# Performance work log

Measured on AMD Instinct MI355X. Metric: run time of the kernel, lower is better.

Reference implementation:

```python
import jax, jax.numpy as jnp
import numpy as np

N = 100_000   # nodes
E = 1_600_000 # edges
IN = 128
OUT = 64
L = 3         # n_layers


def setup_inputs() -> dict:
    key = jax.random.key(0)
    ks = jax.random.split(key, 4)
    x = jax.random.normal(ks[0], (N, IN), dtype=jnp.float32)
    edge_index = jax.random.randint(ks[1], (2, E), 0, N, dtype=jnp.int64)
    # Glorot-ish init like torch Linear default
    s0 = 1.0 / np.sqrt(IN)
    W0 = jax.random.uniform(ks[2], (IN, OUT), jnp.float32, -s0, s0)
    b0 = jnp.zeros((OUT,), jnp.float32)
    so = 1.0 / np.sqrt(OUT)
    Ws = jax.random.uniform(ks[3], (L - 1, OUT, OUT), jnp.float32, -so, so)
    bs = jnp.zeros((L - 1, OUT), jnp.float32)
    return {"x": x, "edge_index": edge_index, "W0": W0, "b0": b0, "Ws": Ws, "bs": bs}


def _gcn_conv(x, src, dst, norm, W, b):
    # dense transform then degree-normalized scatter-add over edges (incl. self-loops)
    h = x @ W                                  # [N, out]
    msg = h[src] * norm[:, None]               # [E+N, out]
    out = jax.ops.segment_sum(msg, dst, num_segments=N)
    return out + b


def reference(x, edge_index, W0, b0, Ws, bs):
    loops = jnp.arange(N, dtype=edge_index.dtype)
    src = jnp.concatenate([edge_index[0], loops])  # source nodes (x_j)
    dst = jnp.concatenate([edge_index[1], loops])  # aggregation targets
    # symmetric GCN normalization: deg over A+I, norm = d^-1/2[src]*d^-1/2[dst]
    deg = jax.ops.segment_sum(jnp.ones(src.shape, x.dtype), dst, num_segments=N)
    dinv = jnp.where(deg > 0, jax.lax.rsqrt(deg), jnp.zeros((), x.dtype))
    norm = dinv[src] * dinv[dst]

    x_temp = _gcn_conv(x, src, dst, norm, W0, b0)
    h = x_temp
    for i in range(L - 1):  # fixed small layer loop
        h = jax.nn.relu(_gcn_conv(h, src, dst, norm, Ws[i], bs[i]))
    return h + x_temp  # sum_res residual
```

## Files before the change

kernel.cpp:

```cpp
#include <hip/hip_runtime.h>


#define LB 8
#define BKN 256
#define CHUNK 2048
#define CAP 8192
#define PADS 3
#define CAPCOL (CAP + BKN * PADS)

typedef unsigned short ushort_t;
typedef __attribute__((ext_vector_type(8))) short bf16x8;
typedef __attribute__((ext_vector_type(4))) float f32x4;

__device__ __forceinline__ unsigned f2bf(float f) {
    unsigned u = __builtin_bit_cast(unsigned, f);
    return (u + 0x7FFFu + ((u >> 16) & 1u)) >> 16;
}
__device__ __forceinline__ float bf2f(ushort_t h) {
    unsigned u = ((unsigned)h) << 16;
    return __builtin_bit_cast(float, u);
}
__device__ __forceinline__ float bflo(unsigned u) {
    return __builtin_bit_cast(float, u << 16);
}
__device__ __forceinline__ float bfhi(unsigned u) {
    return __builtin_bit_cast(float, u & 0xFFFF0000u);
}

__device__ int detect_f64(const int* ei, int E, int* sflag) {
    if (threadIdx.x == 0) *sflag = 0;
    __syncthreads();
    const unsigned* raw = (const unsigned*)ei;
    int dwords = min(2 * E, 4096);
    int any = 0;
    for (int i = threadIdx.x; i < dwords; i += blockDim.x)
        if ((i & 1) && raw[i]) any = 1;
    if (any) atomicOr(sflag, 1);
    __syncthreads();
    return !*sflag;
}

__global__ __launch_bounds__(256) void k_scatter(
        const int* __restrict__ ei, int E,
        int* __restrict__ bucketCursor, unsigned int* __restrict__ packed) {
    __shared__ int hist[512];
    __shared__ int base[512];
    __shared__ int sflag;
    int f64 = detect_f64(ei, E, &sflag);
    int b0 = blockIdx.x * CHUNK;
    int n = min(CHUNK, E - b0);
    for (int i = threadIdx.x; i < 512; i += 256) hist[i] = 0;
    __syncthreads();
    for (int i = threadIdx.x; i < n; i += 256) {
        int e = b0 + i;
        int d = f64 ? ei[2 * (E + e)] : ei[E + e];
        atomicAdd(&hist[d >> LB], 1);
    }
    __syncthreads();
    for (int i = threadIdx.x; i < 512; i += 256) {
        int c = hist[i];
        base[i] = c ? atomicAdd(&bucketCursor[i], c) : 0;
        hist[i] = 0;
    }
    __syncthreads();
    for (int i = threadIdx.x; i < n; i += 256) {
        int e = b0 + i;
        int d = f64 ? ei[2 * (E + e)] : ei[E + e];
        int s = f64 ? ei[2 * e] : ei[e];
        int bk = d >> LB;
        int pos = bk * CAP + base[bk] + atomicAdd(&hist[bk], 1);
        packed[pos] = ((unsigned)s << LB) | (unsigned)(d & (BKN - 1));
    }
}

__global__ __launch_bounds__(256) void k_sort(
        const unsigned int* __restrict__ packed, const int* __restrict__ bucketCursor,
        int* __restrict__ col, int2* __restrict__ rp2, float* __restrict__ dinv,
        ushort_t* __restrict__ hs, int N) {
    __shared__ int hist[BKN];
    __shared__ int s[BKN];
    __shared__ int cur[BKN];
    int tid = threadIdx.x;
    int b = blockIdx.x;
    int start = b * CAP;
    int end = start + bucketCursor[b];
    hist[tid] = 0;
    __syncthreads();
    for (int e = start + tid; e < end; e += 256)
        atomicAdd(&hist[packed[e] & (BKN - 1)], 1);
    __syncthreads();
    int v = hist[tid];
    int pv = (v + PADS) & ~PADS;
    s[tid] = pv;
    __syncthreads();
    for (int off = 1; off < 256; off <<= 1) {
        int x = (tid >= off) ? s[tid - off] : 0;
        __syncthreads();
        if (tid >= off) s[tid] += x;
        __syncthreads();
    }
    int excl = s[tid] - pv;
    int st = b * CAPCOL + excl;
    cur[tid] = st;
    int node = (b << LB) + tid;
    if (node < N) {
        rp2[node] = make_int2(st, st + pv);
        dinv[node] = rsqrtf((float)(v + 1));
        for (int i = v; i < pv; i++) col[st + i] = N;
    }
    if (b == 0 && tid < 64) hs[(size_t)N * 64 + tid] = 0;
    __syncthreads();
    for (int e = start + tid; e < end; e += 256) {
        unsigned pvk = packed[e];
        int pos = atomicAdd(&cur[pvk & (BKN - 1)], 1);
        col[pos] = (int)(pvk >> LB);
    }
}

__global__ __launch_bounds__(256) void k_gemm1(
        const float* __restrict__ A, const float* __restrict__ W,
        const float* __restrict__ dinv, ushort_t* __restrict__ out, int nrows) {
    const int K = 128;
    __shared__ ushort_t sWT[64 * (K + 8)];
    int tid = threadIdx.x;
    for (int i = tid; i < K * 64; i += 256) {
        int n = i & 63, k = i >> 6;
        sWT[n * (K + 8) + k] = (ushort_t)f2bf(W[i]);
    }
    __syncthreads();
    int wave = tid >> 6, lane = tid & 63;
    int quad = lane >> 4, l16 = lane & 15;
    int rowBase = blockIdx.x * 128 + wave * 32;
    f32x4 acc[2][4];
#pragma unroll
    for (int r = 0; r < 2; r++)
#pragma unroll
        for (int c = 0; c < 4; c++) acc[r][c] = (f32x4){0.f, 0.f, 0.f, 0.f};
#pragma unroll
    for (int chunk = 0; chunk < K / 32; chunk++) {
        bf16x8 afr[2];
#pragma unroll
        for (int r = 0; r < 2; r++) {
            int row = rowBase + r * 16 + l16;
            if (row >= nrows) row = nrows - 1;
            const float* ap = A + (size_t)row * K + chunk * 32 + quad * 8;
            float4 v0 = *(const float4*)ap;
            float4 v1 = *(const float4*)(ap + 4);
            bf16x8 a;
            a[0] = (short)f2bf(v0.x); a[1] = (short)f2bf(v0.y);
            a[2] = (short)f2bf(v0.z); a[3] = (short)f2bf(v0.w);
            a[4] = (short)f2bf(v1.x); a[5] = (short)f2bf(v1.y);
            a[6] = (short)f2bf(v1.z); a[7] = (short)f2bf(v1.w);
            afr[r] = a;
        }
#pragma unroll
        for (int c = 0; c < 4; c++) {
            bf16x8 bfr = __builtin_bit_cast(
                bf16x8,
                *(const uint4*)&sWT[(c * 16 + l16) * (K + 8) + chunk * 32 + quad * 8]);
#pragma unroll
            for (int r = 0; r < 2; r++)
                acc[r][c] = __builtin_amdgcn_mfma_f32_16x16x32_bf16(
                    afr[r], bfr, acc[r][c], 0, 0, 0);
        }
    }
#pragma unroll
    for (int r = 0; r < 2; r++)
#pragma unroll
        for (int i = 0; i < 4; i++) {
            int row = rowBase + r * 16 + quad * 4 + i;
            if (row < nrows) {
                float sc = dinv[row];
#pragma unroll
                for (int c = 0; c < 4; c++)
                    out[(size_t)row * 64 + c * 16 + l16] =
                        (ushort_t)f2bf(acc[r][c][i] * sc);
            }
        }
}

__global__ __launch_bounds__(256) void k_gemm64(
        const ushort_t* __restrict__ A, const float* __restrict__ W,
        const float* __restrict__ dinv, ushort_t* __restrict__ out, int nrows) {
    const int K = 64;
    __shared__ ushort_t sWT[64 * (K + 8)];
    int tid = threadIdx.x;
    for (int i = tid; i < K * 64; i += 256) {
        int n = i & 63, k = i >> 6;
        sWT[n * (K + 8) + k] = (ushort_t)f2bf(W[i]);
    }
    __syncthreads();
    int wave = tid >> 6, lane = tid & 63;
    int quad = lane >> 4, l16 = lane & 15;
    int rowBase = blockIdx.x * 128 + wave * 32;
    f32x4 acc[2][4];
#pragma unroll
    for (int r = 0; r < 2; r++)
#pragma unroll
        for (int c = 0; c < 4; c++) acc[r][c] = (f32x4){0.f, 0.f, 0.f, 0.f};
#pragma unroll
    for (int chunk = 0; chunk < K / 32; chunk++) {
        bf16x8 afr[2];
#pragma unroll
        for (int r = 0; r < 2; r++) {
            int row = rowBase + r * 16 + l16;
            if (row >= nrows) row = nrows - 1;
            const ushort_t* ap = A + (size_t)row * K + chunk * 32 + quad * 8;
            afr[r] = __builtin_bit_cast(bf16x8, *(const uint4*)ap);
        }
#pragma unroll
        for (int c = 0; c < 4; c++) {
            bf16x8 bfr = __builtin_bit_cast(
                bf16x8,
                *(const uint4*)&sWT[(c * 16 + l16) * (K + 8) + chunk * 32 + quad * 8]);
#pragma unroll
            for (int r = 0; r < 2; r++)
                acc[r][c] = __builtin_amdgcn_mfma_f32_16x16x32_bf16(
                    afr[r], bfr, acc[r][c], 0, 0, 0);
        }
    }
#pragma unroll
    for (int r = 0; r < 2; r++)
#pragma unroll
        for (int i = 0; i < 4; i++) {
            int row = rowBase + r * 16 + quad * 4 + i;
            if (row < nrows) {
                float sc = dinv[row];
#pragma unroll
                for (int c = 0; c < 4; c++)
                    out[(size_t)row * 64 + c * 16 + l16] =
                        (ushort_t)f2bf(acc[r][c][i] * sc);
            }
        }
}

template <int RELU, int F32OUT>
__global__ __launch_bounds__(256) void k_agg4e(
        const ushort_t* __restrict__ hs, const float* __restrict__ dinv,
        const float* __restrict__ bias, const int* __restrict__ col,
        const int2* __restrict__ rp2, const ushort_t* __restrict__ residb,
        float* __restrict__ outf, ushort_t* __restrict__ outb, int n) {
    int node = (int)((blockIdx.x * blockDim.x + threadIdx.x) >> 6);
    if (node >= n) return;
    int lane = threadIdx.x & 63;
    int g = lane >> 4;
    int c4 = lane & 15;
    const ushort_t* hrow = hs + (size_t)c4 * 4;
    int2 r = rp2[node];
    int e = r.x, p = r.y;
    uint2 us = *(const uint2*)(hs + (size_t)node * 64 + c4 * 4);
    float a0 = 0.f, a1 = 0.f, a2 = 0.f, a3 = 0.f;

#define GR(m) (*(const uint2*)(hrow + (size_t)(m) * 64))
#define GACC(u)                                                             \
    a0 += bflo(u.x); a1 += bfhi(u.x);                                       \
    a2 += bflo(u.y); a3 += bfhi(u.y);

    for (; e + 16 <= p; e += 16) {
        int m0 = col[e + g];
        int m1 = col[e + 4 + g];
        int m2 = col[e + 8 + g];
        int m3 = col[e + 12 + g];
        uint2 u0 = GR(m0);
        uint2 u1 = GR(m1);
        uint2 u2 = GR(m2);
        uint2 u3 = GR(m3);
        GACC(u0) GACC(u1) GACC(u2) GACC(u3)
    }
    if (p - e >= 8) {
        int m0 = col[e + g];
        int m1 = col[e + 4 + g];
        uint2 u0 = GR(m0);
        uint2 u1 = GR(m1);
        GACC(u0) GACC(u1)
        e += 8;
    }
    if (e < p) {
        int m0 = col[e + g];
        uint2 u0 = GR(m0);
        GACC(u0)
    }
#undef GR
#undef GACC

    a0 += __shfl_xor(a0, 16); a0 += __shfl_xor(a0, 32);
    a1 += __shfl_xor(a1, 16); a1 += __shfl_xor(a1, 32);
    a2 += __shfl_xor(a2, 16); a2 += __shfl_xor(a2, 32);
    a3 += __shfl_xor(a3, 16); a3 += __shfl_xor(a3, 32);

    if (lane < 16) {
        a0 += bflo(us.x); a1 += bfhi(us.x);
        a2 += bflo(us.y); a3 += bfhi(us.y);
        float sc = dinv[node];
        float4 bv = *(const float4*)(bias + c4 * 4);
        float o0 = sc * a0 + bv.x, o1 = sc * a1 + bv.y;
        float o2 = sc * a2 + bv.z, o3 = sc * a3 + bv.w;
        if (RELU) {
            o0 = fmaxf(o0, 0.f); o1 = fmaxf(o1, 0.f);
            o2 = fmaxf(o2, 0.f); o3 = fmaxf(o3, 0.f);
        }
        if (F32OUT) {
            uint2 rb = *(const uint2*)(residb + (size_t)node * 64 + c4 * 4);
            o0 += bflo(rb.x); o1 += bfhi(rb.x);
            o2 += bflo(rb.y); o3 += bfhi(rb.y);
            *(float4*)(outf + (size_t)node * 64 + c4 * 4) =
                make_float4(o0, o1, o2, o3);
        } else {
            unsigned w0 = f2bf(o0) | (f2bf(o1) << 16);
            unsigned w1 = f2bf(o2) | (f2bf(o3) << 16);
            *(uint2*)(outb + (size_t)node * 64 + c4 * 4) = make_uint2(w0, w1);
        }
    }
}

extern "C" void kernel_launch(void* const* d_in, const int* in_sizes, int n_in,
                              void* d_out, int out_size, void* d_ws, size_t ws_size,
                              hipStream_t stream) {
    const float* x  = (const float*)d_in[0];
    const int*   ei = (const int*)d_in[1];
    const float* W0 = (const float*)d_in[2];
    const float* b0 = (const float*)d_in[3];
    const float* Ws = (const float*)d_in[4];
    const float* bs = (const float*)d_in[5];
    float* out = (float*)d_out;

    const int N = in_sizes[0] / 128;
    const int E = in_sizes[1] / 2;
    const int B = (N + BKN - 1) >> LB;

    char* p = (char*)d_ws;
    auto carve = [&](size_t bytes) {
        char* r = p;
        p += (bytes + 255) & ~(size_t)255;
        return r;
    };
    int*      bucketCursor = (int*)carve(512 * 4);
    unsigned* packed       = (unsigned*)carve((size_t)B * CAP * 4);
    int*      col          = (int*)carve(((size_t)B * CAPCOL + 64) * 4);
    int2*     rp2          = (int2*)carve((size_t)N * 8);
    float*    dinv         = (float*)carve((size_t)N * 4);
    ushort_t* hs           = (ushort_t*)carve((size_t)(N + 1) * 64 * 2);
    ushort_t* xtb          = (ushort_t*)carve((size_t)N * 64 * 2);
    ushort_t* hb           = (ushort_t*)carve((size_t)N * 64 * 2);

    hipMemsetAsync(bucketCursor, 0, 512 * 4, stream);

    k_scatter<<<(E + CHUNK - 1) / CHUNK, 256, 0, stream>>>(ei, E, bucketCursor, packed);
    k_sort<<<B, 256, 0, stream>>>(packed, bucketCursor, col, rp2, dinv, hs, N);

    int gb = (N + 127) / 128;
    int ablocks = (N + 3) / 4;

    k_gemm1<<<gb, 256, 0, stream>>>(x, W0, dinv, hs, N);
    k_agg4e<0, 0><<<ablocks, 256, 0, stream>>>(hs, dinv, b0, col, rp2,
                                               nullptr, nullptr, xtb, N);
    k_gemm64<<<gb, 256, 0, stream>>>(xtb, Ws, dinv, hs, N);
    k_agg4e<1, 0><<<ablocks, 256, 0, stream>>>(hs, dinv, bs, col, rp2,
                                               nullptr, nullptr, hb, N);
    k_gemm64<<<gb, 256, 0, stream>>>(hb, Ws + 64 * 64, dinv, hs, N);
    k_agg4e<1, 1><<<ablocks, 256, 0, stream>>>(hs, dinv, bs + 64, col, rp2,
                                               xtb, out, nullptr, N);
}
```

Measured before the change: 308.7 us.

## Replace two-level bucket sort CSR build with degree count, scan, and fill

The CSR construction moves from a bucketed scatter plus per-bucket shared-memory sort to three kernels. The first counts degrees with global atomics, the second scans per 256-node block to get row starts and dinv, and the third places each edge with a global atomic cursor per destination. This drops the packed intermediate buffer and one full pass over it. The cost is heavy contention on global atomics spread across random addresses, and neighbor order within a row becomes nondeterministic. The f64 detection sample is also shrunk.

```diff
diff --git a/kernel.cpp b/kernel.cpp
--- a/kernel.cpp
+++ b/kernel.cpp
@@ -3,7 +3,6 @@
 
 #define LB 8
 #define BKN 256
-#define CHUNK 2048
 #define CAP 8192
 #define PADS 3
 #define CAPCOL (CAP + BKN * PADS)
@@ -31,7 +30,7 @@
     if (threadIdx.x == 0) *sflag = 0;
     __syncthreads();
     const unsigned* raw = (const unsigned*)ei;
-    int dwords = min(2 * E, 4096);
+    int dwords = min(2 * E, 512);
     int any = 0;
     for (int i = threadIdx.x; i < dwords; i += blockDim.x)
         if ((i & 1) && raw[i]) any = 1;
@@ -40,56 +39,26 @@
     return !*sflag;
 }
 
-__global__ __launch_bounds__(256) void k_scatter(
-        const int* __restrict__ ei, int E,
-        int* __restrict__ bucketCursor, unsigned int* __restrict__ packed) {
-    __shared__ int hist[512];
-    __shared__ int base[512];
+__global__ __launch_bounds__(256) void k_deg(
+        const int* __restrict__ ei, int E, int* __restrict__ deg) {
     __shared__ int sflag;
     int f64 = detect_f64(ei, E, &sflag);
-    int b0 = blockIdx.x * CHUNK;
-    int n = min(CHUNK, E - b0);
-    for (int i = threadIdx.x; i < 512; i += 256) hist[i] = 0;
-    __syncthreads();
-    for (int i = threadIdx.x; i < n; i += 256) {
-        int e = b0 + i;
+    int stride = gridDim.x * 256;
+    for (int e = blockIdx.x * 256 + threadIdx.x; e < E; e += stride) {
         int d = f64 ? ei[2 * (E + e)] : ei[E + e];
-        atomicAdd(&hist[d >> LB], 1);
-    }
-    __syncthreads();
-    for (int i = threadIdx.x; i < 512; i += 256) {
-        int c = hist[i];
-        base[i] = c ? atomicAdd(&bucketCursor[i], c) : 0;
-        hist[i] = 0;
-    }
-    __syncthreads();
-    for (int i = threadIdx.x; i < n; i += 256) {
-        int e = b0 + i;
-        int d = f64 ? ei[2 * (E + e)] : ei[E + e];
-        int s = f64 ? ei[2 * e] : ei[e];
-        int bk = d >> LB;
-        int pos = bk * CAP + base[bk] + atomicAdd(&hist[bk], 1);
-        packed[pos] = ((unsigned)s << LB) | (unsigned)(d & (BKN - 1));
-    }
-}
-
-__global__ __launch_bounds__(256) void k_sort(
-        const unsigned int* __restrict__ packed, const int* __restrict__ bucketCursor,
-        int* __restrict__ col, int2* __restrict__ rp2, float* __restrict__ dinv,
+        atomicAdd(&deg[d], 1);
+    }
+}
+
+__global__ __launch_bounds__(256) void k_scan(
+        const int* __restrict__ deg, int* __restrict__ cur, int* __restrict__ col,
+        int2* __restrict__ rp2, float* __restrict__ dinv,
         ushort_t* __restrict__ hs, int N) {
-    __shared__ int hist[BKN];
     __shared__ int s[BKN];
-    __shared__ int cur[BKN];
     int tid = threadIdx.x;
     int b = blockIdx.x;
-    int start = b * CAP;
-    int end = start + bucketCursor[b];
-    hist[tid] = 0;
-    __syncthreads();
-    for (int e = start + tid; e < end; e += 256)
-        atomicAdd(&hist[packed[e] & (BKN - 1)], 1);
-    __syncthreads();
-    int v = hist[tid];
+    int node = (b << LB) + tid;
+    int v = (node < N) ? deg[node] : 0;
     int pv = (v + PADS) & ~PADS;
     s[tid] = pv;
     __syncthreads();
@@ -99,21 +68,27 @@
         if (tid >= off) s[tid] += x;
         __syncthreads();
     }
-    int excl = s[tid] - pv;
-    int st = b * CAPCOL + excl;
-    cur[tid] = st;
-    int node = (b << LB) + tid;
+    int st = b * CAPCOL + s[tid] - pv;
     if (node < N) {
         rp2[node] = make_int2(st, st + pv);
         dinv[node] = rsqrtf((float)(v + 1));
+        cur[node] = st;
         for (int i = v; i < pv; i++) col[st + i] = N;
     }
     if (b == 0 && tid < 64) hs[(size_t)N * 64 + tid] = 0;
-    __syncthreads();
-    for (int e = start + tid; e < end; e += 256) {
-        unsigned pvk = packed[e];
-        int pos = atomicAdd(&cur[pvk & (BKN - 1)], 1);
-        col[pos] = (int)(pvk >> LB);
+}
+
+__global__ __launch_bounds__(256) void k_fill(
+        const int* __restrict__ ei, int E,
+        int* __restrict__ cur, int* __restrict__ col) {
+    __shared__ int sflag;
+    int f64 = detect_f64(ei, E, &sflag);
+    int stride = gridDim.x * 256;
+    for (int e = blockIdx.x * 256 + threadIdx.x; e < E; e += stride) {
+        int d = f64 ? ei[2 * (E + e)] : ei[E + e];
+        int s = f64 ? ei[2 * e] : ei[e];
+        int pos = atomicAdd(&cur[d], 1);
+        col[pos] = s;
     }
 }
 
@@ -334,19 +309,21 @@
         p += (bytes + 255) & ~(size_t)255;
         return r;
     };
-    int*      bucketCursor = (int*)carve(512 * 4);
-    unsigned* packed       = (unsigned*)carve((size_t)B * CAP * 4);
-    int*      col          = (int*)carve(((size_t)B * CAPCOL + 64) * 4);
-    int2*     rp2          = (int2*)carve((size_t)N * 8);
-    float*    dinv         = (float*)carve((size_t)N * 4);
-    ushort_t* hs           = (ushort_t*)carve((size_t)(N + 1) * 64 * 2);
-    ushort_t* xtb          = (ushort_t*)carve((size_t)N * 64 * 2);
-    ushort_t* hb           = (ushort_t*)carve((size_t)N * 64 * 2);
-
-    hipMemsetAsync(bucketCursor, 0, 512 * 4, stream);
-
-    k_scatter<<<(E + CHUNK - 1) / CHUNK, 256, 0, stream>>>(ei, E, bucketCursor, packed);
-    k_sort<<<B, 256, 0, stream>>>(packed, bucketCursor, col, rp2, dinv, hs, N);
+    int*      deg  = (int*)carve((size_t)N * 4);
+    int*      cur  = (int*)carve((size_t)N * 4);
+    int*      col  = (int*)carve(((size_t)B * CAPCOL + 64) * 4);
+    int2*     rp2  = (int2*)carve((size_t)N * 8);
+    float*    dinv = (float*)carve((size_t)N * 4);
+    ushort_t* hs   = (ushort_t*)carve((size_t)(N + 1) * 64 * 2);
+    ushort_t* xtb  = (ushort_t*)carve((size_t)N * 64 * 2);
+    ushort_t* hb   = (ushort_t*)carve((size_t)N * 64 * 2);
+
+    hipMemsetAsync(deg, 0, (size_t)N * 4, stream);
+
+    int eb = min((E + 255) / 256, 2048);
+    k_deg<<<eb, 256, 0, stream>>>(ei, E, deg);
+    k_scan<<<B, 256, 0, stream>>>(deg, cur, col, rp2, dinv, hs, N);
+    k_fill<<<eb, 256, 0, stream>>>(ei, E, cur, col);
 
     int gb = (N + 127) / 128;
     int ablocks = (N + 3) / 4;
```

After: 473.6 us. 1.53x slower.
